# Performance work log

Hardware: AMD Instinct MI355X
Metric: run time of the kernel (lower is better)

Reference implementation:

```python
import jax, jax.numpy as jnp
import numpy as np

EPS = 1e-5
N_HEADS = 16

def _bn(x, g, b, m, v):
    # x: (N,C,L); inference-mode batchnorm with running stats
    scale = g * jax.lax.rsqrt(v + EPS)
    return (x - m[None, :, None]) * scale[None, :, None] + b[None, :, None]

def _conv1d(x, w, b, pad):
    # x: (N,C,L), w: (O,I,K) torch layout
    y = jax.lax.conv_general_dilated(x, w, window_strides=(1,), padding=[(pad, pad)],
                                     dimension_numbers=('NCH', 'OIH', 'NCH'))
    return y + b[None, :, None]

def _instance_norm(x):
    m = x.mean(-1, keepdims=True)
    v = x.var(-1, keepdims=True)
    return (x - m) * jax.lax.rsqrt(v + EPS)

def setup_inputs() -> dict:
    key = jax.random.key(0)
    ks = jax.random.split(key, 12)
    C, MID, N, L = 1024, 1024, 4, 1024
    s = 0.02
    d = {
        'x': jax.random.normal(ks[0], (N, C, L), jnp.float32),
        'norm_g': jnp.ones((C,), jnp.float32) + 0.1 * jax.random.normal(ks[1], (C,)),
        'norm_b': 0.1 * jax.random.normal(ks[2], (C,)),
        'norm_m': 0.05 * jax.random.normal(ks[3], (C,)),
        'norm_v': jnp.ones((C,), jnp.float32),
        'wq': s * jax.random.normal(ks[4], (C, C)),
        'wk': s * jax.random.normal(ks[5], (C, C)),
        'wv': s * jax.random.normal(ks[6], (C, C)),
        'wo': s * jax.random.normal(ks[7], (C, C)),
        'cw1': s * jax.random.normal(ks[8], (MID, C, 1)),
        'cb1': jnp.zeros((MID,), jnp.float32),
        'cw2': s * jax.random.normal(ks[9], (MID, MID, 3)),
        'cb2': jnp.zeros((MID,), jnp.float32),
        'cw3': s * jax.random.normal(ks[10], (C, MID, 1)),
        'cb3': jnp.zeros((C,), jnp.float32),
    }
    for i, cdim in [(1, MID), (2, MID), (3, C)]:
        kk = jax.random.split(ks[11], 8)
        d[f'bn{i}_g'] = jnp.ones((cdim,), jnp.float32) + 0.1 * jax.random.normal(kk[2 * i - 2], (cdim,))
        d[f'bn{i}_b'] = 0.1 * jax.random.normal(kk[2 * i - 1], (cdim,))
        d[f'bn{i}_m'] = 0.05 * jax.random.normal(jax.random.fold_in(key, 100 + i), (cdim,))
        d[f'bn{i}_v'] = jnp.ones((cdim,), jnp.float32)
    return d

def _attention(h, wq, wk, wv, wo):
    # h: (N,L,C) ; torch Linear: y = x @ W.T
    N, L, C = h.shape
    dh = C // N_HEADS
    q = (h @ wq.T).reshape(N, L, N_HEADS, dh)
    k = (h @ wk.T).reshape(N, L, N_HEADS, dh)
    v = (h @ wv.T).reshape(N, L, N_HEADS, dh)
    att = jnp.einsum('nqhd,nkhd->nhqk', q, k) / jnp.sqrt(jnp.float32(C))  # note: /sqrt(d_model) as in source
    att = jax.nn.softmax(att, axis=-1)
    o = jnp.einsum('nhqk,nkhd->nqhd', att, v).reshape(N, L, C)
    return o @ wo.T

def _forward(x, norm_g, norm_b, norm_m, norm_v, wq, wk, wv, wo,
             cw1, cb1, bn1_g, bn1_b, bn1_m, bn1_v,
             cw2, cb2, bn2_g, bn2_b, bn2_m, bn2_v,
             cw3, cb3, bn3_g, bn3_b, bn3_m, bn3_v):
    # self-attention branch (dropout is identity in eval)
    h = _bn(x, norm_g, norm_b, norm_m, norm_v).transpose(0, 2, 1)  # (N,L,C)
    h = h + _attention(h, wq, wk, wv, wo)
    h = h.transpose(0, 2, 1)  # (N,C,L)
    # IbnNet (bottleneck conv block + residual + optional InstanceNorm)
    y = jax.nn.relu(_bn(_conv1d(h, cw1, cb1, 0), bn1_g, bn1_b, bn1_m, bn1_v))
    y = jax.nn.relu(_bn(_conv1d(y, cw2, cb2, 1), bn2_g, bn2_b, bn2_m, bn2_v))
    y = _bn(_conv1d(y, cw3, cb3, 0), bn3_g, bn3_b, bn3_m, bn3_v)
    y = jax.nn.relu(_instance_norm(y + h))
    # max_pool1d(kernel=2, stride=2)
    N, C, L = y.shape
    return y.reshape(N, C, L // 2, 2).max(axis=-1)

def reference(x, norm_g, norm_b, norm_m, norm_v, wq, wk, wv, wo,
              cw1, cb1, bn1_g, bn1_b, bn1_m, bn1_v,
              cw2, cb2, bn2_g, bn2_b, bn2_m, bn2_v,
              cw3, cb3, bn3_g, bn3_b, bn3_m, bn3_v):
    return _forward(x, norm_g, norm_b, norm_m, norm_v, wq, wk, wv, wo,
                    cw1, cb1, bn1_g, bn1_b, bn1_m, bn1_v,
                    cw2, cb2, bn2_g, bn2_b, bn2_m, bn2_v,
                    cw3, cb3, bn3_g, bn3_b, bn3_m, bn3_v)
```

## Files before the change

kernel.cpp:

```cpp
#include <hip/hip_runtime.h>
#include <cstdint>
#include <cstddef>


typedef __bf16 bf16_t;
typedef __attribute__((ext_vector_type(8))) __bf16 bf16x8;
typedef __attribute__((ext_vector_type(4))) __bf16 bf16x4;
typedef __attribute__((ext_vector_type(4))) float f32x4;
typedef __attribute__((ext_vector_type(8))) unsigned short u16x8;
typedef __attribute__((address_space(1))) unsigned int gu32;
typedef __attribute__((address_space(3))) unsigned int lu32;

#define EPSF 1e-5f

__device__ __forceinline__ void glds16(const void* g, void* l) {
  __builtin_amdgcn_global_load_lds((gu32*)g, (lu32*)l, 16, 0, 0);
}

__device__ __forceinline__ f32x4 mfma16(bf16x8 a, bf16x8 b, f32x4 c) {
  return __builtin_amdgcn_mfma_f32_16x16x32_bf16(a, b, c, 0, 0, 0);
}

__global__ void bn_consts_k(const float* __restrict__ g, const float* __restrict__ b,
                            const float* __restrict__ m, const float* __restrict__ v,
                            const float* __restrict__ cb,
                            float* __restrict__ sc, float* __restrict__ sh, int C) {
  int i = blockIdx.x * 256 + threadIdx.x;
  if (i < C) {
    float s = g[i] * rsqrtf(v[i] + EPSF);
    sc[i] = s;
    sh[i] = b[i] + ((cb ? cb[i] : 0.f) - m[i]) * s;
  }
}

__global__ __launch_bounds__(256)
void bn_transpose_k(const float* __restrict__ x, const float* __restrict__ sc,
                    const float* __restrict__ sh, float* __restrict__ H0f,
                    bf16_t* __restrict__ H0b) {
  __shared__ float T[32][33];
  const int n = blockIdx.x, c0 = blockIdx.y * 32, l0 = blockIdx.z * 32;
  const int tx = threadIdx.x & 31, ty = threadIdx.x >> 5;
#pragma unroll
  for (int cc = 0; cc < 4; ++cc) {
    int c = c0 + ty + cc * 8;
    float v = x[((size_t)(n * 1024 + c) << 10) + l0 + tx];
    T[ty + cc * 8][tx] = v * sc[c] + sh[c];
  }
  __syncthreads();
#pragma unroll
  for (int cc = 0; cc < 4; ++cc) {
    int l = l0 + ty + cc * 8;
    float v = T[tx][ty + cc * 8];
    size_t idx = ((size_t)(n * 1024 + l) << 10) + c0 + tx;
    H0f[idx] = v;
    H0b[idx] = (bf16_t)v;
  }
}

__global__ void cast6_k(const float* __restrict__ s0, const float* __restrict__ s1,
                        const float* __restrict__ s2, const float* __restrict__ s3,
                        const float* __restrict__ s4, const float* __restrict__ s5,
                        bf16_t* __restrict__ d0, bf16_t* __restrict__ d1,
                        bf16_t* __restrict__ d2, bf16_t* __restrict__ d3,
                        bf16_t* __restrict__ d4, bf16_t* __restrict__ d5) {
  const int b = blockIdx.x, which = b >> 10;
  const int i = (b & 1023) * 256 + threadIdx.x;
  const float* s; bf16_t* d;
  switch (which) {
    case 0: s = s0; d = d0; break;
    case 1: s = s1; d = d1; break;
    case 2: s = s2; d = d2; break;
    case 3: s = s3; d = d3; break;
    case 4: s = s4; d = d4; break;
    default: s = s5; d = d5; break;
  }
  f32x4 v = *(const f32x4*)(s + (size_t)i * 4);
  bf16x4 o;
  o[0] = (bf16_t)v[0]; o[1] = (bf16_t)v[1]; o[2] = (bf16_t)v[2]; o[3] = (bf16_t)v[3];
  *(bf16x4*)(d + (size_t)i * 4) = o;
}

__global__ void pack_w2_k(const float* __restrict__ s, bf16_t* __restrict__ d) {
  int i = blockIdx.x * 256 + threadIdx.x;
  int o = i / 3072;
  int r = i - o * 3072;
  int c = r / 3;
  int k = r - c * 3;
  d[(size_t)o * 3072 + k * 1024 + c] = (bf16_t)s[i];
}

__global__ void build_a2_k(const bf16_t* __restrict__ Y1, bf16_t* __restrict__ A2) {
  int t = blockIdx.x * 256 + threadIdx.x;
  int i = t / 384;
  int qq = t - i * 384;
  int tap = qq >> 7;
  int c8 = (qq & 127) * 8;
  int l = i & 1023;
  int ll = l + tap - 1;
  u16x8 val = {0, 0, 0, 0, 0, 0, 0, 0};
  if ((unsigned)ll < 1024u) val = *(const u16x8*)(Y1 + (size_t)(i + tap - 1) * 1024 + c8);
  *(u16x8*)(A2 + (size_t)i * 3072 + tap * 1024 + c8) = val;
}

__global__ __launch_bounds__(256)
void gemm_nt(const bf16_t* __restrict__ A, const bf16_t* __restrict__ B, int K,
             int nNT, int qkv, float alpha, const float* __restrict__ bnScale,
             const float* __restrict__ bnShift, int doRelu,
             const float* __restrict__ resid, float* __restrict__ outF,
             bf16_t* __restrict__ outB) {
  __shared__ __align__(16) bf16_t As[2][128 * 64];
  __shared__ __align__(16) bf16_t Bs[2][64 * 64];

  const int bid = blockIdx.x;
  const int wg = (bid & 7) * (gridDim.x >> 3) + (bid >> 3);
  const int mt = wg / nNT, nt = wg - mt * nNT;
  const int tileM = mt * 128, tileN = nt * 64;

  const int tid = threadIdx.x;
  const int lane = tid & 63;
  const int w = tid >> 6, wr = w >> 1, wc = w & 1;
  const int l16 = lane & 15, g = lane >> 4;

  const bf16_t* aSrc[4];
  const bf16_t* bSrc[2];
#pragma unroll
  for (int it = 0; it < 4; ++it) {
    int q = it * 256 + tid, r = q >> 3, s = q & 7;
    aSrc[it] = A + (size_t)(tileM + r) * K + ((s ^ (r & 7)) * 8);
  }
#pragma unroll
  for (int it = 0; it < 2; ++it) {
    int q = it * 256 + tid, r = q >> 3, s = q & 7;
    bSrc[it] = B + (size_t)(tileN + r) * K + ((s ^ (r & 7)) * 8);
  }

  f32x4 acc[4][2];
#pragma unroll
  for (int m = 0; m < 4; ++m)
#pragma unroll
    for (int n = 0; n < 2; ++n) acc[m][n] = {0.f, 0.f, 0.f, 0.f};

#pragma unroll
  for (int it = 0; it < 4; ++it) glds16(aSrc[it], &As[0][(it * 256 + tid) * 8]);
#pragma unroll
  for (int it = 0; it < 2; ++it) glds16(bSrc[it], &Bs[0][(it * 256 + tid) * 8]);
  __syncthreads();

  int buf = 0;
  for (int k0 = 0; k0 < K; k0 += 64) {
    if (k0 + 64 < K) {
#pragma unroll
      for (int it = 0; it < 4; ++it)
        glds16(aSrc[it] + k0 + 64, &As[buf ^ 1][(it * 256 + tid) * 8]);
#pragma unroll
      for (int it = 0; it < 2; ++it)
        glds16(bSrc[it] + k0 + 64, &Bs[buf ^ 1][(it * 256 + tid) * 8]);
    }
#pragma unroll
    for (int kk = 0; kk < 2; ++kk) {
      bf16x8 af[4], bfr[2];
#pragma unroll
      for (int m = 0; m < 4; ++m) {
        int r = wr * 64 + m * 16 + l16;
        af[m] = *(const bf16x8*)(&As[buf][r * 64 + (((kk * 4 + g) ^ (r & 7)) * 8)]);
      }
#pragma unroll
      for (int n = 0; n < 2; ++n) {
        int r = wc * 32 + n * 16 + l16;
        bfr[n] = *(const bf16x8*)(&Bs[buf][r * 64 + (((kk * 4 + g) ^ (r & 7)) * 8)]);
      }
#pragma unroll
      for (int m = 0; m < 4; ++m)
#pragma unroll
        for (int n = 0; n < 2; ++n) acc[m][n] = mfma16(af[m], bfr[n], acc[m][n]);
    }
    __syncthreads();
    buf ^= 1;
  }

#pragma unroll
  for (int m = 0; m < 4; ++m) {
#pragma unroll
    for (int n = 0; n < 2; ++n) {
#pragma unroll
      for (int j = 0; j < 4; ++j) {
        const int gr = tileM + wr * 64 + m * 16 + g * 4 + j;
        const int gc = tileN + wc * 32 + n * 16 + l16;
        if (qkv) {
          const int which = gc >> 10, c = gc & 1023;
          float v = acc[m][n][j] * (which == 0 ? 0.03125f : 1.f);
          if (which == 2)
            outB[8388608 + ((size_t)(gr >> 10) << 20) + ((size_t)c << 10) + (gr & 1023)] =
                (bf16_t)v;
          else
            outB[(size_t)which * 4194304 + ((size_t)gr << 10) + c] = (bf16_t)v;
        } else {
          float v = acc[m][n][j] * alpha;
          if (bnScale) v = v * bnScale[gc] + bnShift[gc];
          if (resid) v += resid[((size_t)gr << 10) + gc];
          if (doRelu) v = fmaxf(v, 0.f);
          if (outF) outF[((size_t)gr << 10) + gc] = v;
          if (outB) outB[((size_t)gr << 10) + gc] = (bf16_t)v;
        }
      }
    }
  }
}

__global__ __launch_bounds__(256)
void attn_fwd(const bf16_t* __restrict__ Qb, const bf16_t* __restrict__ Kb,
              const bf16_t* __restrict__ Vt, bf16_t* __restrict__ AO) {
  __shared__ __align__(16) bf16_t Ks[2][64][64];
  __shared__ __align__(16) bf16_t Vs[2][64][64];
  __shared__ __align__(16) bf16_t Ps[4][2][16][64];

  const int bid = blockIdx.x;
  const int xcd = bid & 7, idx = bid >> 3;
  const int head = xcd * 8 + (idx >> 3);
  const int qblk = idx & 7;
  const int n = head >> 4, h = head & 15;

  const int tid = threadIdx.x, lane = tid & 63, w = tid >> 6;
  const int l16 = lane & 15, g = lane >> 4;
  const int qbase = qblk * 128 + w * 32;

  bf16x8 aq[2][2];
#pragma unroll
  for (int s = 0; s < 2; ++s) {
    const size_t qoff = ((size_t)(n * 1024 + qbase + s * 16 + l16) << 10) + h * 64;
    aq[s][0] = *(const bf16x8*)(Qb + qoff + g * 8);
    aq[s][1] = *(const bf16x8*)(Qb + qoff + 32 + g * 8);
  }

  const bf16_t* Khead = Kb + ((size_t)(n * 1024) << 10) + h * 64;
  const bf16_t* Vhead = Vt + ((size_t)n << 20) + ((size_t)(h * 64) << 10);

  f32x4 oa[2][4];
  float psum[2][4];
#pragma unroll
  for (int s = 0; s < 2; ++s)
#pragma unroll
    for (int i = 0; i < 4; ++i) {
      oa[s][i] = {0.f, 0.f, 0.f, 0.f};
      psum[s][i] = 0.f;
    }

#pragma unroll
  for (int it = 0; it < 2; ++it) {
    int q = it * 256 + tid, r = q >> 3, c = q & 7;
    glds16(Khead + ((size_t)r << 10) + ((c ^ (r & 7)) * 8), &Ks[0][r][c * 8]);
    glds16(Vhead + ((size_t)r << 10) + ((c ^ (r & 7)) * 8), &Vs[0][r][c * 8]);
  }
  asm volatile("s_waitcnt vmcnt(0)" ::: "memory");
  __syncthreads();

  int buf = 0;
  for (int t = 0; t < 16; ++t) {
    if (t < 15) {
      const int kv0 = (t + 1) * 64;
#pragma unroll
      for (int it = 0; it < 2; ++it) {
        int q = it * 256 + tid, r = q >> 3, c = q & 7;
        glds16(Khead + ((size_t)(kv0 + r) << 10) + ((c ^ (r & 7)) * 8),
               &Ks[buf ^ 1][r][c * 8]);
        glds16(Vhead + ((size_t)r << 10) + kv0 + ((c ^ (r & 7)) * 8),
               &Vs[buf ^ 1][r][c * 8]);
      }
    }
    bf16x8 kf[8];
#pragma unroll
    for (int nf = 0; nf < 4; ++nf) {
      const int r = nf * 16 + l16;
      kf[2 * nf]     = *(const bf16x8*)(&Ks[buf][r][((g)     ^ (r & 7)) * 8]);
      kf[2 * nf + 1] = *(const bf16x8*)(&Ks[buf][r][((4 + g) ^ (r & 7)) * 8]);
    }
#pragma unroll
    for (int s = 0; s < 2; ++s) {
      f32x4 sc[4];
#pragma unroll
      for (int nf = 0; nf < 4; ++nf) sc[nf] = {0.f, 0.f, 0.f, 0.f};
#pragma unroll
      for (int nf = 0; nf < 4; ++nf) {
        sc[nf] = mfma16(aq[s][0], kf[2 * nf], sc[nf]);
        sc[nf] = mfma16(aq[s][1], kf[2 * nf + 1], sc[nf]);
      }
#pragma unroll
      for (int nf = 0; nf < 4; ++nf)
#pragma unroll
        for (int j = 0; j < 4; ++j) {
          float p = __expf(sc[nf][j]);
          psum[s][j] += p;
          const int row = g * 4 + j;
          const int ch = (nf * 2 + (l16 >> 3)) ^ (row & 7);
          Ps[w][s][row][ch * 8 + (l16 & 7)] = (bf16_t)p;
        }
    }
    bf16x8 vf[8];
#pragma unroll
    for (int nf = 0; nf < 4; ++nf) {
      const int r = nf * 16 + l16;
      vf[2 * nf]     = *(const bf16x8*)(&Vs[buf][r][((g)     ^ (r & 7)) * 8]);
      vf[2 * nf + 1] = *(const bf16x8*)(&Vs[buf][r][((4 + g) ^ (r & 7)) * 8]);
    }
#pragma unroll
    for (int s = 0; s < 2; ++s)
#pragma unroll
      for (int kk = 0; kk < 2; ++kk) {
        const int ch = (kk * 4 + g) ^ (l16 & 7);
        bf16x8 pa = *(const bf16x8*)(&Ps[w][s][l16][ch * 8]);
#pragma unroll
        for (int nf = 0; nf < 4; ++nf)
          oa[s][nf] = mfma16(pa, vf[2 * nf + kk], oa[s][nf]);
      }
    asm volatile("s_waitcnt vmcnt(0)" ::: "memory");
    __syncthreads();
    buf ^= 1;
  }

#pragma unroll
  for (int s = 0; s < 2; ++s)
#pragma unroll
    for (int j = 0; j < 4; ++j) {
      float sv = psum[s][j];
#pragma unroll
      for (int o = 1; o < 16; o <<= 1) sv += __shfl_xor(sv, o);
      psum[s][j] = sv;
    }
#pragma unroll
  for (int s = 0; s < 2; ++s)
#pragma unroll
    for (int nf = 0; nf < 4; ++nf)
#pragma unroll
      for (int j = 0; j < 4; ++j) {
        const int q = qbase + s * 16 + g * 4 + j;
        AO[((size_t)(n * 1024 + q) << 10) + h * 64 + nf * 16 + l16] =
            (bf16_t)(oa[s][nf][j] / psum[s][j]);
      }
}

__global__ void in_stats_k(const float* __restrict__ Z, float* __restrict__ ps,
                           float* __restrict__ pq) {
  const int n = blockIdx.x, c = blockIdx.y * 256 + threadIdx.x, z = blockIdx.z;
  float s = 0.f, s2 = 0.f;
  for (int i = 0; i < 128; ++i) {
    float v = Z[((size_t)(n * 1024 + z * 128 + i) << 10) + c];
    s += v;
    s2 += v * v;
  }
  ps[z * 4096 + n * 1024 + c] = s;
  pq[z * 4096 + n * 1024 + c] = s2;
}

__global__ __launch_bounds__(256)
void finalize_k(const float* __restrict__ Z, const float* __restrict__ ps,
                const float* __restrict__ pq, float* __restrict__ out) {
  __shared__ float T[32][33];
  const int n = blockIdx.x, c0 = blockIdx.y * 32, j0 = blockIdx.z * 32;
  const int tx = threadIdx.x & 31, ty = threadIdx.x >> 5;
  const int c = c0 + tx;
  float s = 0.f, q = 0.f;
#pragma unroll
  for (int z = 0; z < 8; ++z) {
    s += ps[z * 4096 + n * 1024 + c];
    q += pq[z * 4096 + n * 1024 + c];
  }
  const float mean = s * (1.f / 1024.f);
  const float var = q * (1.f / 1024.f) - mean * mean;
  const float rstd = rsqrtf(var + EPSF);
#pragma unroll
  for (int jj = 0; jj < 4; ++jj) {
    const int j = j0 + ty + jj * 8;
    float a = Z[((size_t)(n * 1024 + 2 * j) << 10) + c];
    float b = Z[((size_t)(n * 1024 + 2 * j + 1) << 10) + c];
    float v = (fmaxf(a, b) - mean) * rstd;
    T[ty + jj * 8][tx] = fmaxf(v, 0.f);
  }
  __syncthreads();
#pragma unroll
  for (int jj = 0; jj < 4; ++jj)
    out[((size_t)(n * 1024 + c0 + ty + jj * 8) << 9) + j0 + tx] = T[tx][ty + jj * 8];
}

extern "C" void kernel_launch(void* const* d_in, const int* in_sizes, int n_in,
                              void* d_out, int out_size, void* d_ws, size_t ws_size,
                              hipStream_t stream) {
  const float* x      = (const float*)d_in[0];
  const float* norm_g = (const float*)d_in[1];
  const float* norm_b = (const float*)d_in[2];
  const float* norm_m = (const float*)d_in[3];
  const float* norm_v = (const float*)d_in[4];
  const float* wq     = (const float*)d_in[5];
  const float* wk     = (const float*)d_in[6];
  const float* wv     = (const float*)d_in[7];
  const float* wo     = (const float*)d_in[8];
  const float* cw1    = (const float*)d_in[9];
  const float* cb1    = (const float*)d_in[10];
  const float* cw2    = (const float*)d_in[11];
  const float* cb2    = (const float*)d_in[12];
  const float* cw3    = (const float*)d_in[13];
  const float* cb3    = (const float*)d_in[14];
  const float* bn1_g  = (const float*)d_in[15];
  const float* bn1_b  = (const float*)d_in[16];
  const float* bn1_m  = (const float*)d_in[17];
  const float* bn1_v  = (const float*)d_in[18];
  const float* bn2_g  = (const float*)d_in[19];
  const float* bn2_b  = (const float*)d_in[20];
  const float* bn2_m  = (const float*)d_in[21];
  const float* bn2_v  = (const float*)d_in[22];
  const float* bn3_g  = (const float*)d_in[23];
  const float* bn3_b  = (const float*)d_in[24];
  const float* bn3_m  = (const float*)d_in[25];
  const float* bn3_v  = (const float*)d_in[26];

  char* ws = (char*)d_ws;
  const size_t MB = 1024 * 1024;
  float*  H0f = (float*)(ws);
  float*  Zf  = H0f;
  float*  H2f = (float*)(ws + 16 * MB);
  bf16_t* H0b = (bf16_t*)(ws + 32 * MB);
  bf16_t* Y2  = H0b;
  bf16_t* Qb  = (bf16_t*)(ws + 40 * MB);
  bf16_t* Kb  = (bf16_t*)(ws + 48 * MB);
  bf16_t* Vt  = (bf16_t*)(ws + 56 * MB);
  bf16_t* A2  = Qb;
  bf16_t* AOb = (bf16_t*)(ws + 64 * MB);
  bf16_t* Y1  = AOb;
  bf16_t* H2b = (bf16_t*)(ws + 72 * MB);
  bf16_t* wqb = (bf16_t*)(ws + 80 * MB);
  bf16_t* wkb = (bf16_t*)(ws + 82 * MB);
  bf16_t* wvb = (bf16_t*)(ws + 84 * MB);
  bf16_t* wob = (bf16_t*)(ws + 86 * MB);
  bf16_t* w1b = (bf16_t*)(ws + 88 * MB);
  bf16_t* w3b = (bf16_t*)(ws + 90 * MB);
  bf16_t* w2b = (bf16_t*)(ws + 92 * MB);
  float* sc0 = (float*)(ws + 98 * MB);
  float* sh0 = sc0 + 1024;
  float* sc1 = sc0 + 2048;
  float* sh1 = sc0 + 3072;
  float* sc2 = sc0 + 4096;
  float* sh2 = sc0 + 5120;
  float* sc3 = sc0 + 6144;
  float* sh3 = sc0 + 7168;
  float* ps  = sc0 + 8192;
  float* pq  = ps + 32768;

  bn_consts_k<<<4, 256, 0, stream>>>(norm_g, norm_b, norm_m, norm_v, nullptr, sc0, sh0, 1024);
  bn_consts_k<<<4, 256, 0, stream>>>(bn1_g, bn1_b, bn1_m, bn1_v, cb1, sc1, sh1, 1024);
  bn_consts_k<<<4, 256, 0, stream>>>(bn2_g, bn2_b, bn2_m, bn2_v, cb2, sc2, sh2, 1024);
  bn_consts_k<<<4, 256, 0, stream>>>(bn3_g, bn3_b, bn3_m, bn3_v, cb3, sc3, sh3, 1024);

  bn_transpose_k<<<dim3(4, 32, 32), 256, 0, stream>>>(x, sc0, sh0, H0f, H0b);

  cast6_k<<<6144, 256, 0, stream>>>(wq, wk, wv, wo, cw1, cw3,
                                    wqb, wkb, wvb, wob, w1b, w3b);
  pack_w2_k<<<12288, 256, 0, stream>>>(cw2, w2b);

  gemm_nt<<<1536, 256, 0, stream>>>(H0b, wqb, 1024, 48, 1, 1.f, nullptr, nullptr, 0,
                                    nullptr, nullptr, Qb);

  attn_fwd<<<512, 256, 0, stream>>>(Qb, Kb, Vt, AOb);

  gemm_nt<<<512, 256, 0, stream>>>(AOb, wob, 1024, 16, 0, 1.f, nullptr, nullptr, 0,
                                   H0f, H2f, H2b);
  gemm_nt<<<512, 256, 0, stream>>>(H2b, w1b, 1024, 16, 0, 1.f, sc1, sh1, 1,
                                   nullptr, nullptr, Y1);
  build_a2_k<<<6144, 256, 0, stream>>>(Y1, A2);
  gemm_nt<<<512, 256, 0, stream>>>(A2, w2b, 3072, 16, 0, 1.f, sc2, sh2, 1,
                                   nullptr, nullptr, Y2);
  gemm_nt<<<512, 256, 0, stream>>>(Y2, w3b, 1024, 16, 0, 1.f, sc3, sh3, 0,
                                   H2f, Zf, nullptr);

  in_stats_k<<<dim3(4, 4, 8), 256, 0, stream>>>(Zf, ps, pq);
  finalize_k<<<dim3(4, 32, 16), 256, 0, stream>>>(Zf, ps, pq, (float*)d_out);
}
```

Measured before the change: 265.0 us.

## Triple-buffer GEMM K-loop with vmcnt waits and drop fp32 H0 copy

The GEMM main loop moves from double buffering with a full __syncthreads to a three-stage LDS ring. It prefetches two tiles ahead and uses explicit s_waitcnt vmcnt plus s_barrier, so global-to-LDS loads overlap more compute. Separately, the batchnorm-transpose kernel no longer writes an fp32 copy of H0, and the output-projection residual reads the bf16 copy instead. This saves 16MB of writes and reads, but the residual now carries bf16 rounding, and the larger LDS footprint may lower occupancy.

```diff
diff --git a/kernel.cpp b/kernel.cpp
--- a/kernel.cpp
+++ b/kernel.cpp
@@ -35,8 +35,7 @@
 
 __global__ __launch_bounds__(256)
 void bn_transpose_k(const float* __restrict__ x, const float* __restrict__ sc,
-                    const float* __restrict__ sh, float* __restrict__ H0f,
-                    bf16_t* __restrict__ H0b) {
+                    const float* __restrict__ sh, bf16_t* __restrict__ H0b) {
   __shared__ float T[32][33];
   const int n = blockIdx.x, c0 = blockIdx.y * 32, l0 = blockIdx.z * 32;
   const int tx = threadIdx.x & 31, ty = threadIdx.x >> 5;
@@ -51,9 +50,7 @@
   for (int cc = 0; cc < 4; ++cc) {
     int l = l0 + ty + cc * 8;
     float v = T[tx][ty + cc * 8];
-    size_t idx = ((size_t)(n * 1024 + l) << 10) + c0 + tx;
-    H0f[idx] = v;
-    H0b[idx] = (bf16_t)v;
+    H0b[((size_t)(n * 1024 + l) << 10) + c0 + tx] = (bf16_t)v;
   }
 }
 
@@ -106,10 +103,10 @@
 void gemm_nt(const bf16_t* __restrict__ A, const bf16_t* __restrict__ B, int K,
              int nNT, int qkv, float alpha, const float* __restrict__ bnScale,
              const float* __restrict__ bnShift, int doRelu,
-             const float* __restrict__ resid, float* __restrict__ outF,
-             bf16_t* __restrict__ outB) {
-  __shared__ __align__(16) bf16_t As[2][128 * 64];
-  __shared__ __align__(16) bf16_t Bs[2][64 * 64];
+             const float* __restrict__ resid, const bf16_t* __restrict__ residB,
+             float* __restrict__ outF, bf16_t* __restrict__ outB) {
+  __shared__ __align__(16) bf16_t As[3][128 * 64];
+  __shared__ __align__(16) bf16_t Bs[3][64 * 64];
 
   const int bid = blockIdx.x;
   const int wg = (bid & 7) * (gridDim.x >> 3) + (bid >> 3);
@@ -140,43 +137,56 @@
 #pragma unroll
     for (int n = 0; n < 2; ++n) acc[m][n] = {0.f, 0.f, 0.f, 0.f};
 
-#pragma unroll
-  for (int it = 0; it < 4; ++it) glds16(aSrc[it], &As[0][(it * 256 + tid) * 8]);
-#pragma unroll
-  for (int it = 0; it < 2; ++it) glds16(bSrc[it], &Bs[0][(it * 256 + tid) * 8]);
-  __syncthreads();
-
-  int buf = 0;
-  for (int k0 = 0; k0 < K; k0 += 64) {
-    if (k0 + 64 < K) {
-#pragma unroll
-      for (int it = 0; it < 4; ++it)
-        glds16(aSrc[it] + k0 + 64, &As[buf ^ 1][(it * 256 + tid) * 8]);
-#pragma unroll
-      for (int it = 0; it < 2; ++it)
-        glds16(bSrc[it] + k0 + 64, &Bs[buf ^ 1][(it * 256 + tid) * 8]);
-    }
+  const int T = K >> 6;
+
+#define STAGE(kt, b)                                                    \
+  {                                                                     \
+    _Pragma("unroll") for (int it = 0; it < 4; ++it)                    \
+        glds16(aSrc[it] + (kt) * 64, &As[b][(it * 256 + tid) * 8]);     \
+    _Pragma("unroll") for (int it = 0; it < 2; ++it)                    \
+        glds16(bSrc[it] + (kt) * 64, &Bs[b][(it * 256 + tid) * 8]);     \
+  }
+
+  STAGE(0, 0);
+  STAGE(1, 1);
+  asm volatile("s_waitcnt vmcnt(6)" ::: "memory");
+  __builtin_amdgcn_s_barrier();
+  __builtin_amdgcn_sched_barrier(0);
+
+  int cur = 0;
+  for (int t = 0; t < T; ++t) {
+    const int nx2 = cur >= 1 ? cur - 1 : 2;
+    if (t + 2 < T) STAGE(t + 2, nx2);
 #pragma unroll
     for (int kk = 0; kk < 2; ++kk) {
       bf16x8 af[4], bfr[2];
 #pragma unroll
       for (int m = 0; m < 4; ++m) {
         int r = wr * 64 + m * 16 + l16;
-        af[m] = *(const bf16x8*)(&As[buf][r * 64 + (((kk * 4 + g) ^ (r & 7)) * 8)]);
+        af[m] = *(const bf16x8*)(&As[cur][r * 64 + (((kk * 4 + g) ^ (r & 7)) * 8)]);
       }
 #pragma unroll
       for (int n = 0; n < 2; ++n) {
         int r = wc * 32 + n * 16 + l16;
-        bfr[n] = *(const bf16x8*)(&Bs[buf][r * 64 + (((kk * 4 + g) ^ (r & 7)) * 8)]);
+        bfr[n] = *(const bf16x8*)(&Bs[cur][r * 64 + (((kk * 4 + g) ^ (r & 7)) * 8)]);
       }
 #pragma unroll
       for (int m = 0; m < 4; ++m)
 #pragma unroll
         for (int n = 0; n < 2; ++n) acc[m][n] = mfma16(af[m], bfr[n], acc[m][n]);
     }
-    __syncthreads();
-    buf ^= 1;
-  }
+    if (t + 1 < T) {
+      if (t + 2 < T) {
+        asm volatile("s_waitcnt vmcnt(6)" ::: "memory");
+      } else {
+        asm volatile("s_waitcnt vmcnt(0)" ::: "memory");
+      }
+      __builtin_amdgcn_s_barrier();
+      __builtin_amdgcn_sched_barrier(0);
+    }
+    cur = cur + 1 >= 3 ? 0 : cur + 1;
+  }
+#undef STAGE
 
 #pragma unroll
   for (int m = 0; m < 4; ++m) {
@@ -198,6 +208,7 @@
           float v = acc[m][n][j] * alpha;
           if (bnScale) v = v * bnScale[gc] + bnShift[gc];
           if (resid) v += resid[((size_t)gr << 10) + gc];
+          if (residB) v += (float)residB[((size_t)gr << 10) + gc];
           if (doRelu) v = fmaxf(v, 0.f);
           if (outF) outF[((size_t)gr << 10) + gc] = v;
           if (outB) outB[((size_t)gr << 10) + gc] = (bf16_t)v;
@@ -414,8 +425,7 @@
 
   char* ws = (char*)d_ws;
   const size_t MB = 1024 * 1024;
-  float*  H0f = (float*)(ws);
-  float*  Zf  = H0f;
+  float*  Zf  = (float*)(ws);
   float*  H2f = (float*)(ws + 16 * MB);
   bf16_t* H0b = (bf16_t*)(ws + 32 * MB);
   bf16_t* Y2  = H0b;
@@ -449,26 +459,26 @@
   bn_consts_k<<<4, 256, 0, stream>>>(bn2_g, bn2_b, bn2_m, bn2_v, cb2, sc2, sh2, 1024);
   bn_consts_k<<<4, 256, 0, stream>>>(bn3_g, bn3_b, bn3_m, bn3_v, cb3, sc3, sh3, 1024);
 
-  bn_transpose_k<<<dim3(4, 32, 32), 256, 0, stream>>>(x, sc0, sh0, H0f, H0b);
+  bn_transpose_k<<<dim3(4, 32, 32), 256, 0, stream>>>(x, sc0, sh0, H0b);
 
   cast6_k<<<6144, 256, 0, stream>>>(wq, wk, wv, wo, cw1, cw3,
                                     wqb, wkb, wvb, wob, w1b, w3b);
   pack_w2_k<<<12288, 256, 0, stream>>>(cw2, w2b);
 
   gemm_nt<<<1536, 256, 0, stream>>>(H0b, wqb, 1024, 48, 1, 1.f, nullptr, nullptr, 0,
-                                    nullptr, nullptr, Qb);
+                                    nullptr, nullptr, nullptr, Qb);
 
   attn_fwd<<<512, 256, 0, stream>>>(Qb, Kb, Vt, AOb);
 
   gemm_nt<<<512, 256, 0, stream>>>(AOb, wob, 1024, 16, 0, 1.f, nullptr, nullptr, 0,
-                                   H0f, H2f, H2b);
+                                   nullptr, H0b, H2f, H2b);
   gemm_nt<<<512, 256, 0, stream>>>(H2b, w1b, 1024, 16, 0, 1.f, sc1, sh1, 1,
-                                   nullptr, nullptr, Y1);
+                                   nullptr, nullptr, nullptr, Y1);
   build_a2_k<<<6144, 256, 0, stream>>>(Y1, A2);
   gemm_nt<<<512, 256, 0, stream>>>(A2, w2b, 3072, 16, 0, 1.f, sc2, sh2, 1,
-                                   nullptr, nullptr, Y2);
+                                   nullptr, nullptr, nullptr, Y2);
   gemm_nt<<<512, 256, 0, stream>>>(Y2, w3b, 1024, 16, 0, 1.f, sc3, sh3, 0,
-                                   H2f, Zf, nullptr);
+                                   H2f, nullptr, Zf, nullptr);
 
   in_stats_k<<<dim3(4, 4, 8), 256, 0, stream>>>(Zf, ps, pq);
   finalize_k<<<dim3(4, 32, 16), 256, 0, stream>>>(Zf, ps, pq, (float*)d_out);
```

New measurement: 277.5 us. +4.7%, slower.

## Fuse im2col construction into conv1 epilogue and use bf16 residual

Applied to the files above, without the earlier changes.

The conv1 GEMM epilogue now scatters each output directly into the three tap slots of the im2col buffer A2, with a small kernel zeroing the padding edges. This removes the separate build_a2 kernel and the Y1 intermediate round trip. The fp32 copy of the normalized input is also dropped, and the attention residual is read from the bf16 copy, which cuts memory traffic but lowers residual precision. The epilogue does three scattered bf16 stores per element.

```diff
diff --git a/kernel.cpp b/kernel.cpp
--- a/kernel.cpp
+++ b/kernel.cpp
@@ -35,8 +35,7 @@
 
 __global__ __launch_bounds__(256)
 void bn_transpose_k(const float* __restrict__ x, const float* __restrict__ sc,
-                    const float* __restrict__ sh, float* __restrict__ H0f,
-                    bf16_t* __restrict__ H0b) {
+                    const float* __restrict__ sh, bf16_t* __restrict__ H0b) {
   __shared__ float T[32][33];
   const int n = blockIdx.x, c0 = blockIdx.y * 32, l0 = blockIdx.z * 32;
   const int tx = threadIdx.x & 31, ty = threadIdx.x >> 5;
@@ -51,9 +50,7 @@
   for (int cc = 0; cc < 4; ++cc) {
     int l = l0 + ty + cc * 8;
     float v = T[tx][ty + cc * 8];
-    size_t idx = ((size_t)(n * 1024 + l) << 10) + c0 + tx;
-    H0f[idx] = v;
-    H0b[idx] = (bf16_t)v;
+    H0b[((size_t)(n * 1024 + l) << 10) + c0 + tx] = (bf16_t)v;
   }
 }
 
@@ -89,25 +86,20 @@
   d[(size_t)o * 3072 + k * 1024 + c] = (bf16_t)s[i];
 }
 
-__global__ void build_a2_k(const bf16_t* __restrict__ Y1, bf16_t* __restrict__ A2) {
-  int t = blockIdx.x * 256 + threadIdx.x;
-  int i = t / 384;
-  int qq = t - i * 384;
-  int tap = qq >> 7;
-  int c8 = (qq & 127) * 8;
-  int l = i & 1023;
-  int ll = l + tap - 1;
-  u16x8 val = {0, 0, 0, 0, 0, 0, 0, 0};
-  if ((unsigned)ll < 1024u) val = *(const u16x8*)(Y1 + (size_t)(i + tap - 1) * 1024 + c8);
-  *(u16x8*)(A2 + (size_t)i * 3072 + tap * 1024 + c8) = val;
+__global__ void zero_a2_edges_k(bf16_t* __restrict__ A2) {
+  int i = blockIdx.x * 256 + threadIdx.x;
+  int n = i >> 11, r = (i >> 10) & 1, c = i & 1023;
+  size_t row = (size_t)(n * 1024 + (r ? 1023 : 0));
+  A2[row * 3072 + (r ? 2048 : 0) + c] = (bf16_t)0.f;
 }
 
 __global__ __launch_bounds__(256)
 void gemm_nt(const bf16_t* __restrict__ A, const bf16_t* __restrict__ B, int K,
              int nNT, int qkv, float alpha, const float* __restrict__ bnScale,
              const float* __restrict__ bnShift, int doRelu,
-             const float* __restrict__ resid, float* __restrict__ outF,
-             bf16_t* __restrict__ outB) {
+             const float* __restrict__ resid, const bf16_t* __restrict__ residB,
+             float* __restrict__ outF, bf16_t* __restrict__ outB,
+             bf16_t* __restrict__ outA2) {
   __shared__ __align__(16) bf16_t As[2][128 * 64];
   __shared__ __align__(16) bf16_t Bs[2][64 * 64];
 
@@ -198,9 +190,17 @@
           float v = acc[m][n][j] * alpha;
           if (bnScale) v = v * bnScale[gc] + bnShift[gc];
           if (resid) v += resid[((size_t)gr << 10) + gc];
+          if (residB) v += (float)residB[((size_t)gr << 10) + gc];
           if (doRelu) v = fmaxf(v, 0.f);
           if (outF) outF[((size_t)gr << 10) + gc] = v;
           if (outB) outB[((size_t)gr << 10) + gc] = (bf16_t)v;
+          if (outA2) {
+            const int l = gr & 1023;
+            const bf16_t bv = (bf16_t)v;
+            outA2[(size_t)gr * 3072 + 1024 + gc] = bv;
+            if (l < 1023) outA2[(size_t)(gr + 1) * 3072 + gc] = bv;
+            if (l > 0) outA2[(size_t)(gr - 1) * 3072 + 2048 + gc] = bv;
+          }
         }
       }
     }
@@ -414,8 +414,7 @@
 
   char* ws = (char*)d_ws;
   const size_t MB = 1024 * 1024;
-  float*  H0f = (float*)(ws);
-  float*  Zf  = H0f;
+  float*  Zf  = (float*)(ws);
   float*  H2f = (float*)(ws + 16 * MB);
   bf16_t* H0b = (bf16_t*)(ws + 32 * MB);
   bf16_t* Y2  = H0b;
@@ -423,9 +422,8 @@
   bf16_t* Kb  = (bf16_t*)(ws + 48 * MB);
   bf16_t* Vt  = (bf16_t*)(ws + 56 * MB);
   bf16_t* A2  = Qb;
+  bf16_t* H2b = (bf16_t*)(ws + 72 * MB);
   bf16_t* AOb = (bf16_t*)(ws + 64 * MB);
-  bf16_t* Y1  = AOb;
-  bf16_t* H2b = (bf16_t*)(ws + 72 * MB);
   bf16_t* wqb = (bf16_t*)(ws + 80 * MB);
   bf16_t* wkb = (bf16_t*)(ws + 82 * MB);
   bf16_t* wvb = (bf16_t*)(ws + 84 * MB);
@@ -449,26 +447,27 @@
   bn_consts_k<<<4, 256, 0, stream>>>(bn2_g, bn2_b, bn2_m, bn2_v, cb2, sc2, sh2, 1024);
   bn_consts_k<<<4, 256, 0, stream>>>(bn3_g, bn3_b, bn3_m, bn3_v, cb3, sc3, sh3, 1024);
 
-  bn_transpose_k<<<dim3(4, 32, 32), 256, 0, stream>>>(x, sc0, sh0, H0f, H0b);
+  bn_transpose_k<<<dim3(4, 32, 32), 256, 0, stream>>>(x, sc0, sh0, H0b);
 
   cast6_k<<<6144, 256, 0, stream>>>(wq, wk, wv, wo, cw1, cw3,
                                     wqb, wkb, wvb, wob, w1b, w3b);
   pack_w2_k<<<12288, 256, 0, stream>>>(cw2, w2b);
 
   gemm_nt<<<1536, 256, 0, stream>>>(H0b, wqb, 1024, 48, 1, 1.f, nullptr, nullptr, 0,
-                                    nullptr, nullptr, Qb);
+                                    nullptr, nullptr, nullptr, Qb, nullptr);
 
   attn_fwd<<<512, 256, 0, stream>>>(Qb, Kb, Vt, AOb);
 
+  zero_a2_edges_k<<<32, 256, 0, stream>>>(A2);
+
   gemm_nt<<<512, 256, 0, stream>>>(AOb, wob, 1024, 16, 0, 1.f, nullptr, nullptr, 0,
-                                   H0f, H2f, H2b);
+                                   nullptr, H0b, H2f, H2b, nullptr);
   gemm_nt<<<512, 256, 0, stream>>>(H2b, w1b, 1024, 16, 0, 1.f, sc1, sh1, 1,
-                                   nullptr, nullptr, Y1);
-  build_a2_k<<<6144, 256, 0, stream>>>(Y1, A2);
+                                   nullptr, nullptr, nullptr, nullptr, A2);
   gemm_nt<<<512, 256, 0, stream>>>(A2, w2b, 3072, 16, 0, 1.f, sc2, sh2, 1,
-                                   nullptr, nullptr, Y2);
+                                   nullptr, nullptr, nullptr, Y2, nullptr);
   gemm_nt<<<512, 256, 0, stream>>>(Y2, w3b, 1024, 16, 0, 1.f, sc3, sh3, 0,
-                                   H2f, Zf, nullptr);
+                                   H2f, nullptr, Zf, nullptr, nullptr);
 
   in_stats_k<<<dim3(4, 4, 8), 256, 0, stream>>>(Zf, ps, pq);
   finalize_k<<<dim3(4, 32, 16), 256, 0, stream>>>(Zf, ps, pq, (float*)d_out);
```

New measurement: 261.8 us. About the same (-1.2%).
